# Performance work log

Hardware: AMD Instinct MI355X
Metric: run time of the kernel (lower is better)

## Reference

```python
import jax, jax.numpy as jnp
import numpy as np

D_MODEL = 1024
NUM_HEADS = 16
D_K = D_MODEL // NUM_HEADS
B, S = 4, 2048


def setup_inputs() -> dict:
    key = jax.random.key(0)
    ks = jax.random.split(key, 11)
    scale = 1.0 / np.sqrt(D_MODEL)
    inp = {
        "query": jax.random.normal(ks[0], (B, S, D_MODEL), dtype=jnp.float32),
        "key": jax.random.normal(ks[1], (B, S, D_MODEL), dtype=jnp.float32),
        "value": jax.random.normal(ks[2], (B, S, D_MODEL), dtype=jnp.float32),
        "mask": jnp.tril(jnp.ones((S, S), dtype=jnp.int32))[None, None, :, :],
        "Wq": jax.random.normal(ks[3], (D_MODEL, D_MODEL), dtype=jnp.float32) * scale,
        "bq": jax.random.normal(ks[4], (D_MODEL,), dtype=jnp.float32) * scale,
        "Wk": jax.random.normal(ks[5], (D_MODEL, D_MODEL), dtype=jnp.float32) * scale,
        "bk": jax.random.normal(ks[6], (D_MODEL,), dtype=jnp.float32) * scale,
        "Wv": jax.random.normal(ks[7], (D_MODEL, D_MODEL), dtype=jnp.float32) * scale,
        "bv": jax.random.normal(ks[8], (D_MODEL,), dtype=jnp.float32) * scale,
        "Wo": jax.random.normal(ks[9], (D_MODEL, D_MODEL), dtype=jnp.float32) * scale,
        "bo": jax.random.normal(ks[10], (D_MODEL,), dtype=jnp.float32) * scale,
    }
    return inp


def reference(query, key, value, mask, Wq, bq, Wk, bk, Wv, bv, Wo, bo):
    b, s, _ = query.shape
    # Linear projections (torch Linear: x @ W.T + b), split into heads -> [B,H,S,Dk]
    Q = (query @ Wq.T + bq).reshape(b, s, NUM_HEADS, D_K).transpose(0, 2, 1, 3)
    K = (key @ Wk.T + bk).reshape(b, s, NUM_HEADS, D_K).transpose(0, 2, 1, 3)
    V = (value @ Wv.T + bv).reshape(b, s, NUM_HEADS, D_K).transpose(0, 2, 1, 3)
    scores = jnp.einsum("bhqd,bhkd->bhqk", Q, K) / jnp.sqrt(jnp.float32(D_K))
    scores = jnp.where(mask == 0, -jnp.inf, scores)
    attn = jax.nn.softmax(scores, axis=-1)  # dropout p=0.0 -> identity
    x = jnp.einsum("bhqk,bhkd->bhqd", attn, V)
    x = x.transpose(0, 2, 1, 3).reshape(b, s, D_MODEL)
    return x @ Wo.T + bo
```

## Files before the change

kernel.cpp:

```cpp
#include <hip/hip_runtime.h>
#include <cstdint>

#define DM   1024
#define NH   16
#define DKd  64
#define Bb   4
#define Ss   2048

using bf16x8_t = __attribute__((ext_vector_type(8))) __bf16;
using bf16x2_t = __attribute__((ext_vector_type(2))) __bf16;
using f32x4_t  = __attribute__((ext_vector_type(4))) float;
using u16x4_t  = __attribute__((ext_vector_type(4))) unsigned short;
using u16x8_t  = __attribute__((ext_vector_type(8))) unsigned short;
using u32x2_t  = __attribute__((ext_vector_type(2))) unsigned int;

#define MFMA16(a, b, c) __builtin_amdgcn_mfma_f32_16x16x32_bf16((a), (b), (c), 0, 0, 0)

__device__ __forceinline__ void mfma_k16(f32x4_t& c, u32x2_t a, u32x2_t b) {
  asm("v_mfma_f32_16x16x16_bf16 %0, %1, %2, %0" : "+v"(c) : "v"(a), "v"(b));
}

__device__ __forceinline__ unsigned short f2bf(float f) {
  union { float f; unsigned u; } v; v.f = f;
  unsigned r = v.u + 0x7fffu + ((v.u >> 16) & 1u);
  return (unsigned short)(r >> 16);
}

__device__ __forceinline__ void gl16(const void* g, void* l) {
  __builtin_amdgcn_global_load_lds(
      (const __attribute__((address_space(1))) void*)g,
      (__attribute__((address_space(3))) void*)l, 16, 0, 0);
}

struct CvtArgs {
  const float* src[4];
  unsigned short* dst[4];
  int n[4];
};

__global__ void cvt_kernel(CvtArgs a) {
  const int seg = blockIdx.y;
  const float* __restrict__ s = a.src[seg];
  unsigned short* __restrict__ d = a.dst[seg];
  const int n = a.n[seg];
  const int step = gridDim.x * blockDim.x * 4;
  for (int i = (blockIdx.x * blockDim.x + threadIdx.x) * 4; i < n; i += step) {
    f32x4_t v = *(const f32x4_t*)(s + i);
    u16x4_t r;
    r[0] = f2bf(v[0]); r[1] = f2bf(v[1]); r[2] = f2bf(v[2]); r[3] = f2bf(v[3]);
    *(u16x4_t*)(d + i) = r;
  }
}

struct GemmArgs {
  const unsigned short* A[3];
  const float* A32[3];
  const unsigned short* W[3];
  const float* bias[3];
  void* out[3];
  float scl[3];
  int epi[3];
};

template <int AMODE>
__global__ __launch_bounds__(256, AMODE ? 3 : 4) void gemm_bt(GemmArgs ga) {
  const int L = blockIdx.x + 8 * (blockIdx.y + 64 * blockIdx.z);
  const int xcd = L & 7;
  const int sidx = L >> 3;
  const int xw = sidx & 7;
  const int grp = sidx >> 3;
  const int z = grp >> 3;
  const int yw = (grp & 7) * 8 + xcd;

  const unsigned short* __restrict__ A = ga.A[z];
  const float* __restrict__ A32 = ga.A32[z];
  const unsigned short* __restrict__ W = ga.W[z];
  const float* __restrict__ bias = ga.bias[z];
  const float scl = ga.scl[z];
  const int epi = ga.epi[z];

  __shared__ __align__(16) unsigned short sA[128 * 32];
  __shared__ __align__(16) unsigned short sB[128 * 32];

  const int tid  = threadIdx.x;
  const int lane = tid & 63;
  const int wid  = tid >> 6;
  const int wm   = wid >> 1, wn = wid & 1;
  const int m0 = yw * 128, n0 = xw * 128;
  const int qr = lane & 15, kg = lane >> 4;

  const int e0 = tid * 8;
  const int e1 = e0 + 2048;
  const int r0 = e0 >> 5, c0 = e0 & 31;
  const int r1 = e1 >> 5, c1 = e1 & 31;

  f32x4_t acc[4][4];
#pragma unroll
  for (int mi = 0; mi < 4; ++mi)
#pragma unroll
    for (int ni = 0; ni < 4; ++ni) acc[mi][ni] = {0.f, 0.f, 0.f, 0.f};

  const float* Ar0 = A32 + (size_t)(m0 + r0) * 1024 + c0;
  const float* Ar1 = A32 + (size_t)(m0 + r1) * 1024 + c1;
  f32x4_t a0l, a0h, a1l, a1h;
  if (AMODE == 1) {
    a0l = *(const f32x4_t*)(Ar0 + 0);
    a0h = *(const f32x4_t*)(Ar0 + 4);
    a1l = *(const f32x4_t*)(Ar1 + 0);
    a1h = *(const f32x4_t*)(Ar1 + 4);
  }

  for (int kt = 0; kt < 32; ++kt) {
    const int k0 = kt * 32;
    if (AMODE == 1) {
      u16x8_t w0, w1;
#pragma unroll
      for (int j = 0; j < 4; ++j) {
        w0[j] = f2bf(a0l[j]); w0[4 + j] = f2bf(a0h[j]);
        w1[j] = f2bf(a1l[j]); w1[4 + j] = f2bf(a1h[j]);
      }
      *(u16x8_t*)&sA[e0] = w0;
      *(u16x8_t*)&sA[e1] = w1;
    } else {
      gl16(A + (size_t)(m0 + r0) * 1024 + k0 + c0, &sA[e0]);
      gl16(A + (size_t)(m0 + r1) * 1024 + k0 + c1, &sA[e1]);
    }
    gl16(W + (size_t)(n0 + r0) * 1024 + k0 + c0, &sB[e0]);
    gl16(W + (size_t)(n0 + r1) * 1024 + k0 + c1, &sB[e1]);
    __syncthreads();

    if (AMODE == 1 && kt + 1 < 32) {
      const int kn = (kt + 1) * 32;
      a0l = *(const f32x4_t*)(Ar0 + kn + 0);
      a0h = *(const f32x4_t*)(Ar0 + kn + 4);
      a1l = *(const f32x4_t*)(Ar1 + kn + 0);
      a1h = *(const f32x4_t*)(Ar1 + kn + 4);
    }

    bf16x8_t af[4], bfr[4];
#pragma unroll
    for (int i = 0; i < 4; ++i) {
      af[i]  = *(const bf16x8_t*)&sA[(wm * 64 + i * 16 + qr) * 32 + kg * 8];
      bfr[i] = *(const bf16x8_t*)&sB[(wn * 64 + i * 16 + qr) * 32 + kg * 8];
    }
#pragma unroll
    for (int mi = 0; mi < 4; ++mi)
#pragma unroll
      for (int ni = 0; ni < 4; ++ni)
        acc[mi][ni] = MFMA16(af[mi], bfr[ni], acc[mi][ni]);
    __syncthreads();
  }

#pragma unroll
  for (int ni = 0; ni < 4; ++ni) {
    const int col = n0 + wn * 64 + ni * 16 + qr;
    const float bi = bias[col];
#pragma unroll
    for (int mi = 0; mi < 4; ++mi) {
      const int mb = m0 + wm * 64 + mi * 16 + kg * 4;
      float vv[4];
#pragma unroll
      for (int j = 0; j < 4; ++j) vv[j] = (acc[mi][ni][j] + bi) * scl;
      if (epi == 0) {
        unsigned short* O = (unsigned short*)ga.out[z];
#pragma unroll
        for (int j = 0; j < 4; ++j) {
          const int m = mb + j;
          O[(size_t)((m >> 11) * NH + (col >> 6)) * (Ss * DKd) +
            (size_t)(m & (Ss - 1)) * DKd + (col & 63)] = f2bf(vv[j]);
        }
      } else if (epi == 2) {
        unsigned short* O = (unsigned short*)ga.out[z];
        u16x4_t r;
#pragma unroll
        for (int j = 0; j < 4; ++j) r[j] = f2bf(vv[j]);
        const int b = mb >> 11, s = mb & (Ss - 1);
        *(u16x4_t*)&O[((size_t)(b * NH + (col >> 6)) * DKd + (col & 63)) * Ss + s] = r;
      } else {
        float* O = (float*)ga.out[z];
#pragma unroll
        for (int j = 0; j < 4; ++j) O[(size_t)(mb + j) * 1024 + col] = vv[j];
      }
    }
  }
}

__global__ __launch_bounds__(256, 5) void attn_kernel(
    const unsigned short* __restrict__ Qp, const unsigned short* __restrict__ Kp,
    const unsigned short* __restrict__ Vt, unsigned short* __restrict__ X) {
  const int x = blockIdx.x, y = blockIdx.y;
  const int bh = (x & 7) * 8 + (y & 7);
  const int pr = (y >> 3) * 4 + (x >> 3);
  const int jsub = 31 - pr;

  const int tid = threadIdx.x, lane = tid & 63, w = tid >> 6;
  const int qr = lane & 15, kg = lane >> 4;

  const unsigned short* Qb = Qp + (size_t)bh * Ss * DKd;
  const unsigned short* Kb = Kp + (size_t)bh * Ss * DKd;
  const unsigned short* Vb = Vt + (size_t)bh * Ss * DKd;

  __shared__ __align__(16) unsigned short kbuf[2][4096];
  __shared__ __align__(16) unsigned short vbuf[2][4096];

  const int R0 = tid >> 3, c80 = (tid & 7) ^ (R0 & 7);
  const int R1 = R0 + 32,  c81 = (tid & 7) ^ (R1 & 7);

  const int bq = bh >> 4, hh = bh & 15;

  const int qbase = jsub * 64;
  const int ntile = jsub + 1;
  const int qrow = qbase + w * 16 + qr;

  const bf16x8_t qf0 = *(const bf16x8_t*)&Qb[(size_t)qrow * DKd + kg * 8];
  const bf16x8_t qf1 = *(const bf16x8_t*)&Qb[(size_t)qrow * DKd + 32 + kg * 8];

  float l_lane = 0.f;
  f32x4_t o[4];
#pragma unroll
  for (int nd = 0; nd < 4; ++nd) o[nd] = {0.f, 0.f, 0.f, 0.f};

  int cur = 0;
  gl16(Kb + (size_t)R0 * DKd + c80 * 8, &kbuf[0][tid * 8]);
  gl16(Kb + (size_t)R1 * DKd + c81 * 8, &kbuf[0][tid * 8 + 2048]);
  gl16(Vb + (size_t)R0 * Ss + c80 * 8, &vbuf[0][tid * 8]);
  gl16(Vb + (size_t)R1 * Ss + c81 * 8, &vbuf[0][tid * 8 + 2048]);
  __syncthreads();

  for (int t = 0; t < ntile; ++t) {
    if (t + 1 < ntile) {
      const int kv0 = (t + 1) * 64;
      const int nb = cur ^ 1;
      gl16(Kb + (size_t)(kv0 + R0) * DKd + c80 * 8, &kbuf[nb][tid * 8]);
      gl16(Kb + (size_t)(kv0 + R1) * DKd + c81 * 8, &kbuf[nb][tid * 8 + 2048]);
      gl16(Vb + (size_t)R0 * Ss + kv0 + c80 * 8, &vbuf[nb][tid * 8]);
      gl16(Vb + (size_t)R1 * Ss + kv0 + c81 * 8, &vbuf[nb][tid * 8 + 2048]);
    }

    f32x4_t s[4];
#pragma unroll
    for (int ni = 0; ni < 4; ++ni) s[ni] = {-8.f, -8.f, -8.f, -8.f};
    __builtin_amdgcn_s_setprio(1);
#pragma unroll
    for (int ni = 0; ni < 4; ++ni) {
      const int R = ni * 16 + qr;
      const bf16x8_t kf0 =
          *(const bf16x8_t*)&kbuf[cur][(R * 8 + (kg ^ (qr & 7))) * 8];
      const bf16x8_t kf1 =
          *(const bf16x8_t*)&kbuf[cur][(R * 8 + ((4 + kg) ^ (qr & 7))) * 8];
      s[ni] = MFMA16(kf0, qf0, s[ni]);
      s[ni] = MFMA16(kf1, qf1, s[ni]);
    }
    __builtin_amdgcn_s_setprio(0);

    if (t == jsub) {
      const int rr = w * 16 + qr;
#pragma unroll
      for (int ni = 0; ni < 4; ++ni)
#pragma unroll
        for (int j = 0; j < 4; ++j)
          if (ni * 16 + kg * 4 + j > rr) s[ni][j] = -1.0e30f;
    }

    float p[4][4];
    float ls = 0.f;
#pragma unroll
    for (int ni = 0; ni < 4; ++ni)
#pragma unroll
      for (int j = 0; j < 4; ++j) {
        p[ni][j] = exp2f(s[ni][j]);
        ls += p[ni][j];
      }
    l_lane += ls;

    u32x2_t pb[4];
#pragma unroll
    for (int c = 0; c < 4; ++c) {
      bf16x2_t lo, hi;
      lo[0] = (__bf16)p[c][0]; lo[1] = (__bf16)p[c][1];
      hi[0] = (__bf16)p[c][2]; hi[1] = (__bf16)p[c][3];
      pb[c][0] = __builtin_bit_cast(unsigned, lo);
      pb[c][1] = __builtin_bit_cast(unsigned, hi);
    }
    asm volatile("s_nop 1");

    __builtin_amdgcn_s_setprio(1);
#pragma unroll
    for (int nd = 0; nd < 4; ++nd) {
      const int rb = (qr + 16 * nd) * 64 + 4 * (kg & 1);
      const int ch = kg >> 1, sw = qr & 7;
      u32x2_t va0 = *(const u32x2_t*)&vbuf[cur][rb + 8 * ((ch + 0) ^ sw)];
      u32x2_t va1 = *(const u32x2_t*)&vbuf[cur][rb + 8 * ((ch + 2) ^ sw)];
      u32x2_t va2 = *(const u32x2_t*)&vbuf[cur][rb + 8 * ((ch + 4) ^ sw)];
      u32x2_t va3 = *(const u32x2_t*)&vbuf[cur][rb + 8 * ((ch + 6) ^ sw)];
      mfma_k16(o[nd], va0, pb[0]);
      mfma_k16(o[nd], va1, pb[1]);
      mfma_k16(o[nd], va2, pb[2]);
      mfma_k16(o[nd], va3, pb[3]);
    }
    __builtin_amdgcn_s_setprio(0);

    __syncthreads();
    cur ^= 1;
  }

  float ls = l_lane;
  ls += __shfl_xor(ls, 16);
  ls += __shfl_xor(ls, 32);
  const float inv = 1.0f / ls;
#pragma unroll
  for (int nd = 0; nd < 4; ++nd) {
    u16x4_t r;
#pragma unroll
    for (int j = 0; j < 4; ++j) r[j] = f2bf(o[nd][j] * inv);
    const int d = nd * 16 + kg * 4;
    *(u16x4_t*)&X[(size_t)(bq * Ss + qrow) * DM + hh * DKd + d] = r;
  }
}

extern "C" void kernel_launch(void* const* d_in, const int* in_sizes, int n_in,
                              void* d_out, int out_size, void* d_ws, size_t ws_size,
                              hipStream_t stream) {
  const float* q  = (const float*)d_in[0];
  const float* k  = (const float*)d_in[1];
  const float* v  = (const float*)d_in[2];
  const float* Wq = (const float*)d_in[4];
  const float* bq = (const float*)d_in[5];
  const float* Wk = (const float*)d_in[6];
  const float* bk = (const float*)d_in[7];
  const float* Wv = (const float*)d_in[8];
  const float* bv = (const float*)d_in[9];
  const float* Wo = (const float*)d_in[10];
  const float* bo = (const float*)d_in[11];

  const size_t NIN = (size_t)Bb * Ss * DM;
  const size_t NW  = (size_t)DM * DM;

  unsigned short* ws  = (unsigned short*)d_ws;
  unsigned short* Wqb = ws;
  unsigned short* Wkb = Wqb + NW;
  unsigned short* Wvb = Wkb + NW;
  unsigned short* Wob = Wvb + NW;
  unsigned short* qb  = Wob + NW;
  unsigned short* Qp  = qb + NIN;
  unsigned short* Kp  = Qp + NIN;
  unsigned short* Vt  = Kp + NIN;
  unsigned short* X   = qb;

  CvtArgs ca{};
  ca.src[0] = Wq; ca.dst[0] = Wqb; ca.n[0] = (int)NW;
  ca.src[1] = Wk; ca.dst[1] = Wkb; ca.n[1] = (int)NW;
  ca.src[2] = Wv; ca.dst[2] = Wvb; ca.n[2] = (int)NW;
  ca.src[3] = Wo; ca.dst[3] = Wob; ca.n[3] = (int)NW;
  cvt_kernel<<<dim3(256, 4), 256, 0, stream>>>(ca);

  const float SC = 0.18033688011112042f;

  GemmArgs g1{};
  g1.A32[0] = q;   g1.A32[1] = k;   g1.A32[2] = v;
  g1.W[0] = Wqb;   g1.W[1] = Wkb;   g1.W[2] = Wvb;
  g1.bias[0] = bq; g1.bias[1] = bk; g1.bias[2] = bv;
  g1.out[0] = Qp;  g1.out[1] = Kp;  g1.out[2] = Vt;
  g1.scl[0] = SC;  g1.scl[1] = 1.f; g1.scl[2] = 1.f;
  g1.epi[0] = 0;   g1.epi[1] = 0;   g1.epi[2] = 2;
  gemm_bt<1><<<dim3(8, 64, 3), 256, 0, stream>>>(g1);

  attn_kernel<<<dim3(32, 64), 256, 0, stream>>>(Qp, Kp, Vt, X);

  GemmArgs g2{};
  g2.A[0] = X; g2.W[0] = Wob; g2.bias[0] = bo; g2.out[0] = d_out;
  g2.scl[0] = 1.f; g2.epi[0] = 1;
  gemm_bt<0><<<dim3(8, 64, 1), 256, 0, stream>>>(g2);
}
```

Before: 182.9 us.

## Pipeline QKV GEMM loads and process 128-row query tiles with paired causal halves

Splits the QKV projection into its own kernel. That kernel double-buffers the weight tiles in LDS and register-prefetches the fp32 activations two steps ahead, using explicit waitcnt and barriers so global loads overlap the MFMA work. The attention kernel now gives each wave 32 query rows (two 16-row groups) that share every K/V tile load, which doubles reuse per LDS read. Each block also handles a pair of causal tiles (15-pr and pr) to balance work across blocks. The cost is higher register pressure (occupancy lowered to 3), fewer blocks (512), and more complex masking on the diagonal tiles.

```diff
diff --git a/kernel.cpp b/kernel.cpp
--- a/kernel.cpp
+++ b/kernel.cpp
@@ -62,8 +62,44 @@
   int epi[3];
 };
 
-template <int AMODE>
-__global__ __launch_bounds__(256, AMODE ? 3 : 4) void gemm_bt(GemmArgs ga) {
+__device__ __forceinline__ void gemm_epilogue(
+    const GemmArgs& ga, int z, int epi, float scl, const float* bias,
+    f32x4_t (&acc)[4][4], int m0, int n0, int wm, int wn, int qr, int kg) {
+#pragma unroll
+  for (int ni = 0; ni < 4; ++ni) {
+    const int col = n0 + wn * 64 + ni * 16 + qr;
+    const float bi = bias[col];
+#pragma unroll
+    for (int mi = 0; mi < 4; ++mi) {
+      const int mb = m0 + wm * 64 + mi * 16 + kg * 4;
+      float vv[4];
+#pragma unroll
+      for (int j = 0; j < 4; ++j) vv[j] = (acc[mi][ni][j] + bi) * scl;
+      if (epi == 0) {
+        unsigned short* O = (unsigned short*)ga.out[z];
+#pragma unroll
+        for (int j = 0; j < 4; ++j) {
+          const int m = mb + j;
+          O[(size_t)((m >> 11) * NH + (col >> 6)) * (Ss * DKd) +
+            (size_t)(m & (Ss - 1)) * DKd + (col & 63)] = f2bf(vv[j]);
+        }
+      } else if (epi == 2) {
+        unsigned short* O = (unsigned short*)ga.out[z];
+        u16x4_t r;
+#pragma unroll
+        for (int j = 0; j < 4; ++j) r[j] = f2bf(vv[j]);
+        const int b = mb >> 11, s = mb & (Ss - 1);
+        *(u16x4_t*)&O[((size_t)(b * NH + (col >> 6)) * DKd + (col & 63)) * Ss + s] = r;
+      } else {
+        float* O = (float*)ga.out[z];
+#pragma unroll
+        for (int j = 0; j < 4; ++j) O[(size_t)(mb + j) * 1024 + col] = vv[j];
+      }
+    }
+  }
+}
+
+__global__ __launch_bounds__(256, 3) void gemm_qkv(GemmArgs ga) {
   const int L = blockIdx.x + 8 * (blockIdx.y + 64 * blockIdx.z);
   const int xcd = L & 7;
   const int sidx = L >> 3;
@@ -72,7 +108,6 @@
   const int z = grp >> 3;
   const int yw = (grp & 7) * 8 + xcd;
 
-  const unsigned short* __restrict__ A = ga.A[z];
   const float* __restrict__ A32 = ga.A32[z];
   const unsigned short* __restrict__ W = ga.W[z];
   const float* __restrict__ bias = ga.bias[z];
@@ -80,7 +115,7 @@
   const int epi = ga.epi[z];
 
   __shared__ __align__(16) unsigned short sA[128 * 32];
-  __shared__ __align__(16) unsigned short sB[128 * 32];
+  __shared__ __align__(16) unsigned short sB[2][128 * 32];
 
   const int tid  = threadIdx.x;
   const int lane = tid & 63;
@@ -102,40 +137,127 @@
 
   const float* Ar0 = A32 + (size_t)(m0 + r0) * 1024 + c0;
   const float* Ar1 = A32 + (size_t)(m0 + r1) * 1024 + c1;
-  f32x4_t a0l, a0h, a1l, a1h;
-  if (AMODE == 1) {
-    a0l = *(const f32x4_t*)(Ar0 + 0);
-    a0h = *(const f32x4_t*)(Ar0 + 4);
-    a1l = *(const f32x4_t*)(Ar1 + 0);
-    a1h = *(const f32x4_t*)(Ar1 + 4);
+
+  f32x4_t areg[2][4];
+
+#define LDA(par, kn)                                        \
+  do {                                                      \
+    areg[par][0] = *(const f32x4_t*)(Ar0 + (kn) * 32 + 0);  \
+    areg[par][1] = *(const f32x4_t*)(Ar0 + (kn) * 32 + 4);  \
+    areg[par][2] = *(const f32x4_t*)(Ar1 + (kn) * 32 + 0);  \
+    areg[par][3] = *(const f32x4_t*)(Ar1 + (kn) * 32 + 4);  \
+  } while (0)
+
+#define WRA(par)                                            \
+  do {                                                      \
+    u16x8_t w0_, w1_;                                       \
+    _Pragma("unroll") for (int j = 0; j < 4; ++j) {         \
+      w0_[j] = f2bf(areg[par][0][j]);                       \
+      w0_[4 + j] = f2bf(areg[par][1][j]);                   \
+      w1_[j] = f2bf(areg[par][2][j]);                       \
+      w1_[4 + j] = f2bf(areg[par][3][j]);                   \
+    }                                                       \
+    *(u16x8_t*)&sA[e0] = w0_;                               \
+    *(u16x8_t*)&sA[e1] = w1_;                               \
+  } while (0)
+
+#define LDW(buf, kn)                                                      \
+  do {                                                                    \
+    gl16(W + (size_t)(n0 + r0) * 1024 + (kn) * 32 + c0, &sB[buf][e0]);    \
+    gl16(W + (size_t)(n0 + r1) * 1024 + (kn) * 32 + c1, &sB[buf][e1]);    \
+  } while (0)
+
+  LDA(0, 0);
+  LDW(0, 0);
+  asm volatile("s_waitcnt vmcnt(2)" ::: "memory");
+  WRA(0);
+  LDA(1, 1);
+  LDW(1, 1);
+  asm volatile("s_waitcnt vmcnt(6)" ::: "memory");
+  asm volatile("s_waitcnt lgkmcnt(0)" ::: "memory");
+  __builtin_amdgcn_s_barrier();
+
+#pragma unroll
+  for (int kt = 0; kt < 32; ++kt) {
+    bf16x8_t af[4], bfr[4];
+#pragma unroll
+    for (int i = 0; i < 4; ++i) {
+      af[i]  = *(const bf16x8_t*)&sA[(wm * 64 + i * 16 + qr) * 32 + kg * 8];
+      bfr[i] = *(const bf16x8_t*)&sB[kt & 1][(wn * 64 + i * 16 + qr) * 32 + kg * 8];
+    }
+    __builtin_amdgcn_s_setprio(1);
+#pragma unroll
+    for (int mi = 0; mi < 4; ++mi)
+#pragma unroll
+      for (int ni = 0; ni < 4; ++ni)
+        acc[mi][ni] = MFMA16(af[mi], bfr[ni], acc[mi][ni]);
+    __builtin_amdgcn_s_setprio(0);
+    __builtin_amdgcn_s_barrier();
+
+    if (kt < 31) {
+      asm volatile("s_waitcnt vmcnt(2)" ::: "memory");
+      WRA((kt + 1) & 1);
+      if (kt + 2 < 32) {
+        LDA(kt & 1, kt + 2);
+        LDW(kt & 1, kt + 2);
+        asm volatile("s_waitcnt vmcnt(6)" ::: "memory");
+      } else {
+        asm volatile("s_waitcnt vmcnt(0)" ::: "memory");
+      }
+      asm volatile("s_waitcnt lgkmcnt(0)" ::: "memory");
+      __builtin_amdgcn_s_barrier();
+    }
   }
+#undef LDA
+#undef WRA
+#undef LDW
+
+  gemm_epilogue(ga, z, epi, scl, bias, acc, m0, n0, wm, wn, qr, kg);
+}
+
+__global__ __launch_bounds__(256, 4) void gemm_bt(GemmArgs ga) {
+  const int L = blockIdx.x + 8 * (blockIdx.y + 64 * blockIdx.z);
+  const int xcd = L & 7;
+  const int sidx = L >> 3;
+  const int xw = sidx & 7;
+  const int grp = sidx >> 3;
+  const int z = grp >> 3;
+  const int yw = (grp & 7) * 8 + xcd;
+
+  const unsigned short* __restrict__ A = ga.A[z];
+  const unsigned short* __restrict__ W = ga.W[z];
+  const float* __restrict__ bias = ga.bias[z];
+  const float scl = ga.scl[z];
+  const int epi = ga.epi[z];
+
+  __shared__ __align__(16) unsigned short sA[128 * 32];
+  __shared__ __align__(16) unsigned short sB[128 * 32];
+
+  const int tid  = threadIdx.x;
+  const int lane = tid & 63;
+  const int wid  = tid >> 6;
+  const int wm   = wid >> 1, wn = wid & 1;
+  const int m0 = yw * 128, n0 = xw * 128;
+  const int qr = lane & 15, kg = lane >> 4;
+
+  const int e0 = tid * 8;
+  const int e1 = e0 + 2048;
+  const int r0 = e0 >> 5, c0 = e0 & 31;
+  const int r1 = e1 >> 5, c1 = e1 & 31;
+
+  f32x4_t acc[4][4];
+#pragma unroll
+  for (int mi = 0; mi < 4; ++mi)
+#pragma unroll
+    for (int ni = 0; ni < 4; ++ni) acc[mi][ni] = {0.f, 0.f, 0.f, 0.f};
 
   for (int kt = 0; kt < 32; ++kt) {
     const int k0 = kt * 32;
-    if (AMODE == 1) {
-      u16x8_t w0, w1;
-#pragma unroll
-      for (int j = 0; j < 4; ++j) {
-        w0[j] = f2bf(a0l[j]); w0[4 + j] = f2bf(a0h[j]);
-        w1[j] = f2bf(a1l[j]); w1[4 + j] = f2bf(a1h[j]);
-      }
-      *(u16x8_t*)&sA[e0] = w0;
-      *(u16x8_t*)&sA[e1] = w1;
-    } else {
-      gl16(A + (size_t)(m0 + r0) * 1024 + k0 + c0, &sA[e0]);
-      gl16(A + (size_t)(m0 + r1) * 1024 + k0 + c1, &sA[e1]);
-    }
+    gl16(A + (size_t)(m0 + r0) * 1024 + k0 + c0, &sA[e0]);
+    gl16(A + (size_t)(m0 + r1) * 1024 + k0 + c1, &sA[e1]);
     gl16(W + (size_t)(n0 + r0) * 1024 + k0 + c0, &sB[e0]);
     gl16(W + (size_t)(n0 + r1) * 1024 + k0 + c1, &sB[e1]);
     __syncthreads();
-
-    if (AMODE == 1 && kt + 1 < 32) {
-      const int kn = (kt + 1) * 32;
-      a0l = *(const f32x4_t*)(Ar0 + kn + 0);
-      a0h = *(const f32x4_t*)(Ar0 + kn + 4);
-      a1l = *(const f32x4_t*)(Ar1 + kn + 0);
-      a1h = *(const f32x4_t*)(Ar1 + kn + 4);
-    }
 
     bf16x8_t af[4], bfr[4];
 #pragma unroll
@@ -151,47 +273,15 @@
     __syncthreads();
   }
 
-#pragma unroll
-  for (int ni = 0; ni < 4; ++ni) {
-    const int col = n0 + wn * 64 + ni * 16 + qr;
-    const float bi = bias[col];
-#pragma unroll
-    for (int mi = 0; mi < 4; ++mi) {
-      const int mb = m0 + wm * 64 + mi * 16 + kg * 4;
-      float vv[4];
-#pragma unroll
-      for (int j = 0; j < 4; ++j) vv[j] = (acc[mi][ni][j] + bi) * scl;
-      if (epi == 0) {
-        unsigned short* O = (unsigned short*)ga.out[z];
-#pragma unroll
-        for (int j = 0; j < 4; ++j) {
-          const int m = mb + j;
-          O[(size_t)((m >> 11) * NH + (col >> 6)) * (Ss * DKd) +
-            (size_t)(m & (Ss - 1)) * DKd + (col & 63)] = f2bf(vv[j]);
-        }
-      } else if (epi == 2) {
-        unsigned short* O = (unsigned short*)ga.out[z];
-        u16x4_t r;
-#pragma unroll
-        for (int j = 0; j < 4; ++j) r[j] = f2bf(vv[j]);
-        const int b = mb >> 11, s = mb & (Ss - 1);
-        *(u16x4_t*)&O[((size_t)(b * NH + (col >> 6)) * DKd + (col & 63)) * Ss + s] = r;
-      } else {
-        float* O = (float*)ga.out[z];
-#pragma unroll
-        for (int j = 0; j < 4; ++j) O[(size_t)(mb + j) * 1024 + col] = vv[j];
-      }
-    }
-  }
-}
-
-__global__ __launch_bounds__(256, 5) void attn_kernel(
+  gemm_epilogue(ga, z, epi, scl, bias, acc, m0, n0, wm, wn, qr, kg);
+}
+
+__global__ __launch_bounds__(256, 3) void attn_kernel(
     const unsigned short* __restrict__ Qp, const unsigned short* __restrict__ Kp,
     const unsigned short* __restrict__ Vt, unsigned short* __restrict__ X) {
   const int x = blockIdx.x, y = blockIdx.y;
-  const int bh = (x & 7) * 8 + (y & 7);
-  const int pr = (y >> 3) * 4 + (x >> 3);
-  const int jsub = 31 - pr;
+  const int bh = x * 8 + (y & 7);
+  const int pr = y >> 3;
 
   const int tid = threadIdx.x, lane = tid & 63, w = tid >> 6;
   const int qr = lane & 15, kg = lane >> 4;
@@ -208,113 +298,142 @@
 
   const int bq = bh >> 4, hh = bh & 15;
 
-  const int qbase = jsub * 64;
-  const int ntile = jsub + 1;
-  const int qrow = qbase + w * 16 + qr;
-
-  const bf16x8_t qf0 = *(const bf16x8_t*)&Qb[(size_t)qrow * DKd + kg * 8];
-  const bf16x8_t qf1 = *(const bf16x8_t*)&Qb[(size_t)qrow * DKd + 32 + kg * 8];
-
-  float l_lane = 0.f;
-  f32x4_t o[4];
-#pragma unroll
-  for (int nd = 0; nd < 4; ++nd) o[nd] = {0.f, 0.f, 0.f, 0.f};
-
-  int cur = 0;
-  gl16(Kb + (size_t)R0 * DKd + c80 * 8, &kbuf[0][tid * 8]);
-  gl16(Kb + (size_t)R1 * DKd + c81 * 8, &kbuf[0][tid * 8 + 2048]);
-  gl16(Vb + (size_t)R0 * Ss + c80 * 8, &vbuf[0][tid * 8]);
-  gl16(Vb + (size_t)R1 * Ss + c81 * 8, &vbuf[0][tid * 8 + 2048]);
-  __syncthreads();
-
-  for (int t = 0; t < ntile; ++t) {
-    if (t + 1 < ntile) {
-      const int kv0 = (t + 1) * 64;
-      const int nb = cur ^ 1;
-      gl16(Kb + (size_t)(kv0 + R0) * DKd + c80 * 8, &kbuf[nb][tid * 8]);
-      gl16(Kb + (size_t)(kv0 + R1) * DKd + c81 * 8, &kbuf[nb][tid * 8 + 2048]);
-      gl16(Vb + (size_t)R0 * Ss + kv0 + c80 * 8, &vbuf[nb][tid * 8]);
-      gl16(Vb + (size_t)R1 * Ss + kv0 + c81 * 8, &vbuf[nb][tid * 8 + 2048]);
-    }
-
-    f32x4_t s[4];
-#pragma unroll
-    for (int ni = 0; ni < 4; ++ni) s[ni] = {-8.f, -8.f, -8.f, -8.f};
-    __builtin_amdgcn_s_setprio(1);
-#pragma unroll
-    for (int ni = 0; ni < 4; ++ni) {
-      const int R = ni * 16 + qr;
-      const bf16x8_t kf0 =
-          *(const bf16x8_t*)&kbuf[cur][(R * 8 + (kg ^ (qr & 7))) * 8];
-      const bf16x8_t kf1 =
-          *(const bf16x8_t*)&kbuf[cur][(R * 8 + ((4 + kg) ^ (qr & 7))) * 8];
-      s[ni] = MFMA16(kf0, qf0, s[ni]);
-      s[ni] = MFMA16(kf1, qf1, s[ni]);
-    }
-    __builtin_amdgcn_s_setprio(0);
-
-    if (t == jsub) {
-      const int rr = w * 16 + qr;
-#pragma unroll
-      for (int ni = 0; ni < 4; ++ni)
-#pragma unroll
-        for (int j = 0; j < 4; ++j)
-          if (ni * 16 + kg * 4 + j > rr) s[ni][j] = -1.0e30f;
-    }
-
-    float p[4][4];
-    float ls = 0.f;
-#pragma unroll
-    for (int ni = 0; ni < 4; ++ni)
+#pragma unroll
+  for (int half = 0; half < 2; ++half) {
+    const int jsub = half == 0 ? (15 - pr) : pr;
+    const int qbase = jsub * 128;
+    const int ntile = 2 * jsub + 2;
+    const int qrowA = qbase + w * 32 + qr;
+    const int qrowB = qrowA + 16;
+
+    const bf16x8_t qfA0 = *(const bf16x8_t*)&Qb[(size_t)qrowA * DKd + kg * 8];
+    const bf16x8_t qfA1 = *(const bf16x8_t*)&Qb[(size_t)qrowA * DKd + 32 + kg * 8];
+    const bf16x8_t qfB0 = *(const bf16x8_t*)&Qb[(size_t)qrowB * DKd + kg * 8];
+    const bf16x8_t qfB1 = *(const bf16x8_t*)&Qb[(size_t)qrowB * DKd + 32 + kg * 8];
+
+    float lA = 0.f, lB = 0.f;
+    f32x4_t o[2][4];
+#pragma unroll
+    for (int g = 0; g < 2; ++g)
+#pragma unroll
+      for (int nd = 0; nd < 4; ++nd) o[g][nd] = {0.f, 0.f, 0.f, 0.f};
+
+    int cur = 0;
+    gl16(Kb + (size_t)R0 * DKd + c80 * 8, &kbuf[0][tid * 8]);
+    gl16(Kb + (size_t)R1 * DKd + c81 * 8, &kbuf[0][tid * 8 + 2048]);
+    gl16(Vb + (size_t)R0 * Ss + c80 * 8, &vbuf[0][tid * 8]);
+    gl16(Vb + (size_t)R1 * Ss + c81 * 8, &vbuf[0][tid * 8 + 2048]);
+    __syncthreads();
+
+    for (int t = 0; t < ntile; ++t) {
+      if (t + 1 < ntile) {
+        const int kv0 = (t + 1) * 64;
+        const int nb = cur ^ 1;
+        gl16(Kb + (size_t)(kv0 + R0) * DKd + c80 * 8, &kbuf[nb][tid * 8]);
+        gl16(Kb + (size_t)(kv0 + R1) * DKd + c81 * 8, &kbuf[nb][tid * 8 + 2048]);
+        gl16(Vb + (size_t)R0 * Ss + kv0 + c80 * 8, &vbuf[nb][tid * 8]);
+        gl16(Vb + (size_t)R1 * Ss + kv0 + c81 * 8, &vbuf[nb][tid * 8 + 2048]);
+      }
+
+      const bool act = !(w < 2 && t == 2 * jsub + 1);
+      if (act) {
+        f32x4_t sA_[4], sB_[4];
+#pragma unroll
+        for (int ni = 0; ni < 4; ++ni) {
+          sA_[ni] = {-8.f, -8.f, -8.f, -8.f};
+          sB_[ni] = {-8.f, -8.f, -8.f, -8.f};
+        }
+        __builtin_amdgcn_s_setprio(1);
+#pragma unroll
+        for (int ni = 0; ni < 4; ++ni) {
+          const int R = ni * 16 + qr;
+          const bf16x8_t kf0 =
+              *(const bf16x8_t*)&kbuf[cur][(R * 8 + (kg ^ (qr & 7))) * 8];
+          const bf16x8_t kf1 =
+              *(const bf16x8_t*)&kbuf[cur][(R * 8 + ((4 + kg) ^ (qr & 7))) * 8];
+          sA_[ni] = MFMA16(kf0, qfA0, sA_[ni]);
+          sA_[ni] = MFMA16(kf1, qfA1, sA_[ni]);
+          sB_[ni] = MFMA16(kf0, qfB0, sB_[ni]);
+          sB_[ni] = MFMA16(kf1, qfB1, sB_[ni]);
+        }
+        __builtin_amdgcn_s_setprio(0);
+
+        if (t >= 2 * jsub) {
+          const int off = (t == 2 * jsub) ? 0 : 64;
+          const int rA = w * 32 + qr - off;
+#pragma unroll
+          for (int ni = 0; ni < 4; ++ni)
+#pragma unroll
+            for (int j = 0; j < 4; ++j) {
+              const int c = ni * 16 + kg * 4 + j;
+              if (c > rA) sA_[ni][j] = -1.0e30f;
+              if (c > rA + 16) sB_[ni][j] = -1.0e30f;
+            }
+        }
+
+        u32x2_t pbA[4], pbB[4];
+#pragma unroll
+        for (int ni = 0; ni < 4; ++ni) {
+          float pa0 = exp2f(sA_[ni][0]), pa1 = exp2f(sA_[ni][1]);
+          float pa2 = exp2f(sA_[ni][2]), pa3 = exp2f(sA_[ni][3]);
+          lA += (pa0 + pa1) + (pa2 + pa3);
+          bf16x2_t lo, hi;
+          lo[0] = (__bf16)pa0; lo[1] = (__bf16)pa1;
+          hi[0] = (__bf16)pa2; hi[1] = (__bf16)pa3;
+          pbA[ni][0] = __builtin_bit_cast(unsigned, lo);
+          pbA[ni][1] = __builtin_bit_cast(unsigned, hi);
+          float pb0 = exp2f(sB_[ni][0]), pb1 = exp2f(sB_[ni][1]);
+          float pb2 = exp2f(sB_[ni][2]), pb3 = exp2f(sB_[ni][3]);
+          lB += (pb0 + pb1) + (pb2 + pb3);
+          bf16x2_t lo2, hi2;
+          lo2[0] = (__bf16)pb0; lo2[1] = (__bf16)pb1;
+          hi2[0] = (__bf16)pb2; hi2[1] = (__bf16)pb3;
+          pbB[ni][0] = __builtin_bit_cast(unsigned, lo2);
+          pbB[ni][1] = __builtin_bit_cast(unsigned, hi2);
+        }
+        asm volatile("s_nop 1");
+
+        __builtin_amdgcn_s_setprio(1);
+#pragma unroll
+        for (int nd = 0; nd < 4; ++nd) {
+          const int rb = (qr + 16 * nd) * 64 + 4 * (kg & 1);
+          const int ch = kg >> 1, sw = qr & 7;
+          u32x2_t va0 = *(const u32x2_t*)&vbuf[cur][rb + 8 * ((ch + 0) ^ sw)];
+          u32x2_t va1 = *(const u32x2_t*)&vbuf[cur][rb + 8 * ((ch + 2) ^ sw)];
+          u32x2_t va2 = *(const u32x2_t*)&vbuf[cur][rb + 8 * ((ch + 4) ^ sw)];
+          u32x2_t va3 = *(const u32x2_t*)&vbuf[cur][rb + 8 * ((ch + 6) ^ sw)];
+          mfma_k16(o[0][nd], va0, pbA[0]);
+          mfma_k16(o[0][nd], va1, pbA[1]);
+          mfma_k16(o[0][nd], va2, pbA[2]);
+          mfma_k16(o[0][nd], va3, pbA[3]);
+          mfma_k16(o[1][nd], va0, pbB[0]);
+          mfma_k16(o[1][nd], va1, pbB[1]);
+          mfma_k16(o[1][nd], va2, pbB[2]);
+          mfma_k16(o[1][nd], va3, pbB[3]);
+        }
+        __builtin_amdgcn_s_setprio(0);
+      }
+
+      __syncthreads();
+      cur ^= 1;
+    }
+
+    float lsA = lA, lsB = lB;
+    lsA += __shfl_xor(lsA, 16); lsA += __shfl_xor(lsA, 32);
+    lsB += __shfl_xor(lsB, 16); lsB += __shfl_xor(lsB, 32);
+    const float invA = 1.0f / lsA, invB = 1.0f / lsB;
+#pragma unroll
+    for (int nd = 0; nd < 4; ++nd) {
+      u16x4_t rA, rB;
 #pragma unroll
       for (int j = 0; j < 4; ++j) {
-        p[ni][j] = exp2f(s[ni][j]);
-        ls += p[ni][j];
+        rA[j] = f2bf(o[0][nd][j] * invA);
+        rB[j] = f2bf(o[1][nd][j] * invB);
       }
-    l_lane += ls;
-
-    u32x2_t pb[4];
-#pragma unroll
-    for (int c = 0; c < 4; ++c) {
-      bf16x2_t lo, hi;
-      lo[0] = (__bf16)p[c][0]; lo[1] = (__bf16)p[c][1];
-      hi[0] = (__bf16)p[c][2]; hi[1] = (__bf16)p[c][3];
-      pb[c][0] = __builtin_bit_cast(unsigned, lo);
-      pb[c][1] = __builtin_bit_cast(unsigned, hi);
-    }
-    asm volatile("s_nop 1");
-
-    __builtin_amdgcn_s_setprio(1);
-#pragma unroll
-    for (int nd = 0; nd < 4; ++nd) {
-      const int rb = (qr + 16 * nd) * 64 + 4 * (kg & 1);
-      const int ch = kg >> 1, sw = qr & 7;
-      u32x2_t va0 = *(const u32x2_t*)&vbuf[cur][rb + 8 * ((ch + 0) ^ sw)];
-      u32x2_t va1 = *(const u32x2_t*)&vbuf[cur][rb + 8 * ((ch + 2) ^ sw)];
-      u32x2_t va2 = *(const u32x2_t*)&vbuf[cur][rb + 8 * ((ch + 4) ^ sw)];
-      u32x2_t va3 = *(const u32x2_t*)&vbuf[cur][rb + 8 * ((ch + 6) ^ sw)];
-      mfma_k16(o[nd], va0, pb[0]);
-      mfma_k16(o[nd], va1, pb[1]);
-      mfma_k16(o[nd], va2, pb[2]);
-      mfma_k16(o[nd], va3, pb[3]);
-    }
-    __builtin_amdgcn_s_setprio(0);
-
-    __syncthreads();
-    cur ^= 1;
-  }
-
-  float ls = l_lane;
-  ls += __shfl_xor(ls, 16);
-  ls += __shfl_xor(ls, 32);
-  const float inv = 1.0f / ls;
-#pragma unroll
-  for (int nd = 0; nd < 4; ++nd) {
-    u16x4_t r;
-#pragma unroll
-    for (int j = 0; j < 4; ++j) r[j] = f2bf(o[nd][j] * inv);
-    const int d = nd * 16 + kg * 4;
-    *(u16x4_t*)&X[(size_t)(bq * Ss + qrow) * DM + hh * DKd + d] = r;
+      const int d = nd * 16 + kg * 4;
+      *(u16x4_t*)&X[(size_t)(bq * Ss + qrowA) * DM + hh * DKd + d] = rA;
+      *(u16x4_t*)&X[(size_t)(bq * Ss + qrowB) * DM + hh * DKd + d] = rB;
+    }
   }
 }
 
@@ -363,12 +482,12 @@
   g1.out[0] = Qp;  g1.out[1] = Kp;  g1.out[2] = Vt;
   g1.scl[0] = SC;  g1.scl[1] = 1.f; g1.scl[2] = 1.f;
   g1.epi[0] = 0;   g1.epi[1] = 0;   g1.epi[2] = 2;
-  gemm_bt<1><<<dim3(8, 64, 3), 256, 0, stream>>>(g1);
-
-  attn_kernel<<<dim3(32, 64), 256, 0, stream>>>(Qp, Kp, Vt, X);
+  gemm_qkv<<<dim3(8, 64, 3), 256, 0, stream>>>(g1);
+
+  attn_kernel<<<dim3(8, 64), 256, 0, stream>>>(Qp, Kp, Vt, X);
 
   GemmArgs g2{};
   g2.A[0] = X; g2.W[0] = Wob; g2.bias[0] = bo; g2.out[0] = d_out;
   g2.scl[0] = 1.f; g2.epi[0] = 1;
-  gemm_bt<0><<<dim3(8, 64, 1), 256, 0, stream>>>(g2);
-}
+  gemm_bt<<<dim3(8, 64, 1), 256, 0, stream>>>(g2);
+}
```

New measurement: 179.2 us. -2.0%, faster.
